# Performance work log

Hardware: AMD Instinct MI355X
Metric: run time of the kernel (lower is better)

## Reference

```python
import jax, jax.numpy as jnp
import numpy as np

D_IN = 1024
D_OUT = 1024
H = 16


def setup_inputs() -> dict:
    key = jax.random.key(0)
    ks = jax.random.split(key, 11)
    B, Tq, Tk = 2, 2048, 2048
    s = 1.0 / np.sqrt(D_IN)
    return {
        "q": jax.random.normal(ks[0], (B, Tq, D_IN), jnp.float32),
        "k": jax.random.normal(ks[1], (B, Tk, D_IN), jnp.float32),
        "v": jax.random.normal(ks[2], (B, Tk, D_IN), jnp.float32),
        "Wq": jax.random.uniform(ks[3], (D_IN, D_OUT), jnp.float32, -s, s),
        "bq": jax.random.uniform(ks[4], (D_OUT,), jnp.float32, -s, s),
        "Wk": jax.random.uniform(ks[5], (D_IN, D_OUT), jnp.float32, -s, s),
        "bk": jax.random.uniform(ks[6], (D_OUT,), jnp.float32, -s, s),
        "Wv": jax.random.uniform(ks[7], (D_IN, D_OUT), jnp.float32, -s, s),
        "bv": jax.random.uniform(ks[8], (D_OUT,), jnp.float32, -s, s),
        "Wo": jax.random.uniform(ks[9], (D_OUT, D_OUT), jnp.float32, -s, s),
        "bo": jax.random.uniform(ks[10], (D_OUT,), jnp.float32, -s, s),
    }


def reference(q, k, v, Wq, bq, Wk, bk, Wv, bv, Wo, bo):
    B, Tq, _ = q.shape
    Tk = k.shape[1]
    hd = D_OUT // H
    # QKV projections, split heads -> [B, H, T, hd]
    qh = (q @ Wq + bq).reshape(B, Tq, H, hd).transpose(0, 2, 1, 3)
    kh = (k @ Wk + bk).reshape(B, Tk, H, hd).transpose(0, 2, 1, 3)
    vh = (v @ Wv + bv).reshape(B, Tk, H, hd).transpose(0, 2, 1, 3)
    # scaled dot-product attention (scale uses key dim = head_dim)
    scores = jnp.einsum("bhqd,bhkd->bhqk", qh, kh) / jnp.sqrt(jnp.float32(hd))
    attn = jax.nn.softmax(scores, axis=-1)
    x = jnp.einsum("bhqk,bhkd->bhqd", attn, vh)
    x = x.transpose(0, 2, 1, 3).reshape(B, Tq, D_OUT)
    return x @ Wo + bo
```

## Files before the change

kernel.cpp:

```cpp
#include <hip/hip_runtime.h>
#include <hip/hip_bf16.h>

typedef __attribute__((ext_vector_type(8))) short short8;
typedef __attribute__((ext_vector_type(4))) short short4v;
typedef __attribute__((ext_vector_type(4))) float f32x4;

__device__ __forceinline__ unsigned short f2bf(float f) {
    __hip_bfloat16 h = __float2bfloat16(f);
    unsigned short u;
    __builtin_memcpy(&u, &h, 2);
    return u;
}
__device__ __forceinline__ short4v pack4bf(float a, float b, float c, float d) {
    union { unsigned u[2]; short4v s; } r;
    r.u[0] = ((unsigned)f2bf(b) << 16) | f2bf(a);
    r.u[1] = ((unsigned)f2bf(d) << 16) | f2bf(c);
    return r.s;
}

#define GLD16(gp, lp) __builtin_amdgcn_global_load_lds( \
    (const __attribute__((address_space(1))) void*)(gp), \
    (__attribute__((address_space(3))) void*)(lp), 16, 0, 0)

__global__ __launch_bounds__(256) void convert3(
    const float* __restrict__ q, const float* __restrict__ k, const float* __restrict__ v,
    unsigned short* __restrict__ qb, unsigned short* __restrict__ kb, unsigned short* __restrict__ vb)
{
    const float* src; unsigned short* dst;
    switch (blockIdx.y) { case 0: src = q; dst = qb; break;
                          case 1: src = k; dst = kb; break;
                          default: src = v; dst = vb; break; }
    size_t i = ((size_t)blockIdx.x * 256 + threadIdx.x) * 8;
    float4 x0 = *(const float4*)&src[i];
    float4 x1 = *(const float4*)&src[i + 4];
    union { unsigned short s[8]; uint4 u; } p;
    p.s[0] = f2bf(x0.x); p.s[1] = f2bf(x0.y); p.s[2] = f2bf(x0.z); p.s[3] = f2bf(x0.w);
    p.s[4] = f2bf(x1.x); p.s[5] = f2bf(x1.y); p.s[6] = f2bf(x1.z); p.s[7] = f2bf(x1.w);
    *(uint4*)&dst[i] = p.u;
}

__global__ __launch_bounds__(256) void transpose_w(
    const float* __restrict__ W0, const float* __restrict__ W1,
    const float* __restrict__ W2, const float* __restrict__ W3,
    unsigned short* __restrict__ T0, unsigned short* __restrict__ T1,
    unsigned short* __restrict__ T2, unsigned short* __restrict__ T3)
{
    __shared__ unsigned short Ts[64 * 72];
    const float* W;
    unsigned short* T;
    switch (blockIdx.z) {
        case 0: W = W0; T = T0; break;
        case 1: W = W1; T = T1; break;
        case 2: W = W2; T = T2; break;
        default: W = W3; T = T3; break;
    }
    int tid = threadIdx.x;
    int c = tid & 7, r = tid >> 3;
    int k0 = blockIdx.x * 64, n0 = blockIdx.y * 64;
    for (int i = 0; i < 64; i += 32) {
        const float* src = &W[(size_t)(k0 + r + i) * 1024 + n0 + c * 8];
        float4 x0 = *(const float4*)src;
        float4 x1 = *(const float4*)(src + 4);
        unsigned short* d = &Ts[(r + i) * 72 + c * 8];
        d[0] = f2bf(x0.x); d[1] = f2bf(x0.y); d[2] = f2bf(x0.z); d[3] = f2bf(x0.w);
        d[4] = f2bf(x1.x); d[5] = f2bf(x1.y); d[6] = f2bf(x1.z); d[7] = f2bf(x1.w);
    }
    __syncthreads();
    for (int i = 0; i < 64; i += 32) {
        union { unsigned short s[8]; uint4 v; } u;
        for (int j = 0; j < 8; j++) u.s[j] = Ts[(c * 8 + j) * 72 + (r + i)];
        *(uint4*)&T[(size_t)(n0 + r + i) * 1024 + k0 + c * 8] = u.v;
    }
}

__device__ __forceinline__ void gemm_core(
    const unsigned short* __restrict__ A, const unsigned short* __restrict__ BT,
    const float* __restrict__ bias, void* __restrict__ outv,
    int mode, float scale)
{
    const int K = 1024;
    __shared__ unsigned short As[2][128 * 32];
    __shared__ unsigned short Bs[2][128 * 32];
    int tid = threadIdx.x;
    int m0 = blockIdx.x * 128, n0 = blockIdx.y * 128;
    int lane = tid & 63, wave = tid >> 6;
    int lm = lane & 15, quad = lane >> 4;
    int wm = (wave >> 1) * 64, wn = (wave & 1) * 64;

    int lrow = lane >> 2, lcol = (lane & 3) * 8;
    const unsigned short* Ag = A + (size_t)(m0 + wave * 32 + lrow) * K + lcol;
    const unsigned short* Bg = BT + (size_t)(n0 + wave * 32 + lrow) * K + lcol;

    f32x4 acc[4][4];
    for (int i = 0; i < 4; i++)
        for (int j = 0; j < 4; j++)
            for (int r = 0; r < 4; r++) acc[i][j][r] = 0.0f;

    GLD16(Ag,          &As[0][(wave * 32) * 32]);
    GLD16(Ag + 16 * K, &As[0][(wave * 32 + 16) * 32]);
    GLD16(Bg,          &Bs[0][(wave * 32) * 32]);
    GLD16(Bg + 16 * K, &Bs[0][(wave * 32 + 16) * 32]);
    __syncthreads();

    for (int it = 0; it < 32; it++) {
        int cur = it & 1;
        if (it < 31) {
            int nxt = cur ^ 1;
            const unsigned short* Agn = Ag + (it + 1) * 32;
            const unsigned short* Bgn = Bg + (it + 1) * 32;
            GLD16(Agn,          &As[nxt][(wave * 32) * 32]);
            GLD16(Agn + 16 * K, &As[nxt][(wave * 32 + 16) * 32]);
            GLD16(Bgn,          &Bs[nxt][(wave * 32) * 32]);
            GLD16(Bgn + 16 * K, &Bs[nxt][(wave * 32 + 16) * 32]);
        }
        short8 a[4], b[4];
        for (int i = 0; i < 4; i++)
            a[i] = *(const short8*)&As[cur][(wm + i * 16 + lm) * 32 + quad * 8];
        for (int j = 0; j < 4; j++)
            b[j] = *(const short8*)&Bs[cur][(wn + j * 16 + lm) * 32 + quad * 8];
        for (int i = 0; i < 4; i++)
            for (int j = 0; j < 4; j++)
                acc[i][j] = __builtin_amdgcn_mfma_f32_16x16x32_bf16(a[i], b[j], acc[i][j], 0, 0, 0);
        __syncthreads();
    }

    for (int j = 0; j < 4; j++) {
        int col = n0 + wn + j * 16 + lm;
        float bv = bias[col];
        for (int i = 0; i < 4; i++) {
            int rowb = m0 + wm + i * 16 + quad * 4;
            if (mode == 0) {
                float* out32 = (float*)outv;
                for (int r = 0; r < 4; r++)
                    out32[(size_t)(rowb + r) * 1024 + col] = (acc[i][j][r] + bv) * scale;
            } else if (mode == 1) {
                unsigned short* out16 = (unsigned short*)outv;
                int h = col >> 6, d = col & 63;
                int bb = rowb >> 11, t = rowb & 2047;
                size_t base = (((size_t)(bb * 16 + h)) * 2048 + t) * 64 + d;
                for (int r = 0; r < 4; r++)
                    out16[base + (size_t)r * 64] = f2bf((acc[i][j][r] + bv) * scale);
            } else {
                unsigned short* out16 = (unsigned short*)outv;
                int h = col >> 6, d = col & 63;
                int bb = rowb >> 11, t = rowb & 2047;
                ushort4 pk;
                pk.x = f2bf((acc[i][j][0] + bv) * scale);
                pk.y = f2bf((acc[i][j][1] + bv) * scale);
                pk.z = f2bf((acc[i][j][2] + bv) * scale);
                pk.w = f2bf((acc[i][j][3] + bv) * scale);
                *(ushort4*)&out16[(((size_t)(bb * 16 + h)) * 64 + d) * 2048 + t] = pk;
            }
        }
    }
}

__global__ __launch_bounds__(256) void qkv_gemm(
    const unsigned short* __restrict__ qbf, const unsigned short* __restrict__ kbf,
    const unsigned short* __restrict__ vbf,
    const unsigned short* __restrict__ WqT, const unsigned short* __restrict__ WkT,
    const unsigned short* __restrict__ WvT,
    const float* __restrict__ bq, const float* __restrict__ bk, const float* __restrict__ bv,
    unsigned short* __restrict__ Qh, unsigned short* __restrict__ Kh,
    unsigned short* __restrict__ VhT)
{
    switch (blockIdx.z) {
        case 0:  gemm_core(qbf, WqT, bq, Qh,  1, 0.18033688011f); break;
        case 1:  gemm_core(kbf, WkT, bk, Kh,  1, 1.0f);           break;
        default: gemm_core(vbf, WvT, bv, VhT, 2, 1.0f);           break;
    }
}

__global__ __launch_bounds__(256) void out_gemm(
    const unsigned short* __restrict__ X, const unsigned short* __restrict__ WoT,
    const float* __restrict__ bo, float* __restrict__ out)
{
    gemm_core(X, WoT, bo, out, 0, 1.0f);
}

__global__ __launch_bounds__(256) void attn_kernel(
    const unsigned short* __restrict__ Qh, const unsigned short* __restrict__ Kh,
    const unsigned short* __restrict__ VhT, unsigned short* __restrict__ X)
{
    __shared__ unsigned short Ks[2][64 * 64];
    __shared__ unsigned short Vt[2][64 * 64];

    int tid = threadIdx.x;
    int qb = blockIdx.x & 31, bh = blockIdx.x >> 5;
    int b = bh >> 4, h = bh & 15;
    int lane = tid & 63, wave = tid >> 6;
    int lm = lane & 15, quad = lane >> 4;

    const unsigned short* Kbase = Kh + (size_t)bh * 2048 * 64;
    const unsigned short* Vbase = VhT + (size_t)bh * 64 * 2048;

    int srow = wave * 8 + (lane >> 3);
    int schk = ((lane & 7) ^ ((lane >> 3) & 7)) * 8;
    int swz  = lm & 7;
    int c0 = (quad ^ swz) * 8;
    int c1 = ((quad + 4) ^ swz) * 8;

    int qrow = qb * 64 + wave * 16 + lm;
    const unsigned short* qptr = Qh + ((size_t)bh * 2048 + qrow) * 64;
    short8 qf0 = *(const short8*)&qptr[quad * 8];
    short8 qf1 = *(const short8*)&qptr[32 + quad * 8];

    f32x4 o[4];
    for (int n = 0; n < 4; n++)
        for (int r = 0; r < 4; r++) o[n][r] = 0.0f;
    float l = 0.0f;

    GLD16(&Kbase[(size_t)srow * 64 + schk],          &Ks[0][(wave * 8) * 64]);
    GLD16(&Kbase[(size_t)(32 + srow) * 64 + schk],   &Ks[0][(32 + wave * 8) * 64]);
    GLD16(&Vbase[(size_t)srow * 2048 + schk],        &Vt[0][(wave * 8) * 64]);
    GLD16(&Vbase[(size_t)(32 + srow) * 2048 + schk], &Vt[0][(32 + wave * 8) * 64]);
    __syncthreads();

    for (int kt = 0; kt < 32; kt++) {
        int cur = kt & 1;
        if (kt < 31) {
            int k1 = (kt + 1) * 64;
            int nxt = cur ^ 1;
            GLD16(&Kbase[(size_t)(k1 + srow) * 64 + schk],        &Ks[nxt][(wave * 8) * 64]);
            GLD16(&Kbase[(size_t)(k1 + 32 + srow) * 64 + schk],   &Ks[nxt][(32 + wave * 8) * 64]);
            GLD16(&Vbase[(size_t)srow * 2048 + k1 + schk],        &Vt[nxt][(wave * 8) * 64]);
            GLD16(&Vbase[(size_t)(32 + srow) * 2048 + k1 + schk], &Vt[nxt][(32 + wave * 8) * 64]);
        }

        short4v pa[4];
        for (int t = 0; t < 4; t++) {
            short8 ka0 = *(const short8*)&Ks[cur][(t * 16 + lm) * 64 + c0];
            short8 ka1 = *(const short8*)&Ks[cur][(t * 16 + lm) * 64 + c1];
            f32x4 z;
            z[0] = z[1] = z[2] = z[3] = 0.0f;
            z = __builtin_amdgcn_mfma_f32_16x16x32_bf16(ka0, qf0, z, 0, 0, 0);
            z = __builtin_amdgcn_mfma_f32_16x16x32_bf16(ka1, qf1, z, 0, 0, 0);
            float p0 = __builtin_amdgcn_exp2f(z[0]);
            float p1 = __builtin_amdgcn_exp2f(z[1]);
            float p2 = __builtin_amdgcn_exp2f(z[2]);
            float p3 = __builtin_amdgcn_exp2f(z[3]);
            l += (p0 + p1) + (p2 + p3);
            pa[t] = pack4bf(p0, p1, p2, p3);
        }

        int wo = (quad & 1) * 4;
        for (int n = 0; n < 4; n++) {
            int rbase = (n * 16 + lm) * 64;
            for (int t = 0; t < 4; t++) {
                int chunk = t * 2 + (quad >> 1);
                short4v vb = *(const short4v*)&Vt[cur][rbase + ((chunk ^ swz) * 8) + wo];
                o[n] = __builtin_amdgcn_mfma_f32_16x16x16bf16_1k(pa[t], vb, o[n], 0, 0, 0);
            }
        }
        __syncthreads();
    }

    l += __shfl_xor(l, 16);
    l += __shfl_xor(l, 32);
    float inv = 1.0f / l;

    for (int r = 0; r < 4; r++) {
        float invr = __shfl(inv, (lane & 48) | (quad * 4 + r));
        int row = qb * 64 + wave * 16 + quad * 4 + r;
        for (int n = 0; n < 4; n++)
            X[((size_t)b * 2048 + row) * 1024 + h * 64 + n * 16 + lm] = f2bf(o[n][r] * invr);
    }
}

extern "C" void kernel_launch(void* const* d_in, const int* in_sizes, int n_in,
                              void* d_out, int out_size, void* d_ws, size_t ws_size,
                              hipStream_t stream)
{
    const float* q  = (const float*)d_in[0];
    const float* k  = (const float*)d_in[1];
    const float* v  = (const float*)d_in[2];
    const float* Wq = (const float*)d_in[3];
    const float* bq = (const float*)d_in[4];
    const float* Wk = (const float*)d_in[5];
    const float* bk = (const float*)d_in[6];
    const float* Wv = (const float*)d_in[7];
    const float* bv = (const float*)d_in[8];
    const float* Wo = (const float*)d_in[9];
    const float* bo = (const float*)d_in[10];

    unsigned short* ws  = (unsigned short*)d_ws;
    const unsigned int M1 = 1u << 20;
    unsigned short* WqT = ws;
    unsigned short* WkT = ws + M1;
    unsigned short* WvT = ws + 2 * M1;
    unsigned short* WoT = ws + 3 * M1;
    unsigned short* qbf = ws + 4 * M1;
    unsigned short* kbf = ws + 8 * M1;
    unsigned short* vbf = ws + 12 * M1;
    unsigned short* Qh  = ws + 16 * M1;
    unsigned short* Kh  = ws + 4 * M1;
    unsigned short* VhT = ws + 8 * M1;
    unsigned short* X   = ws + 12 * M1;

    convert3<<<dim3(2048, 3), 256, 0, stream>>>(q, k, v, qbf, kbf, vbf);
    transpose_w<<<dim3(16, 16, 4), 256, 0, stream>>>(Wq, Wk, Wv, Wo, WqT, WkT, WvT, WoT);
    qkv_gemm<<<dim3(32, 8, 3), 256, 0, stream>>>(qbf, kbf, vbf, WqT, WkT, WvT,
                                                 bq, bk, bv, Qh, Kh, VhT);
    attn_kernel<<<dim3(1024), 256, 0, stream>>>(Qh, Kh, VhT, X);
    out_gemm<<<dim3(32, 8), 256, 0, stream>>>(X, WoT, bo, (float*)d_out);
}
```

Baseline: 247.7 us.

## Merge prep kernels and swizzle single-buffered GEMM shared-memory tiles

Fuses the bf16 input conversion and weight transpose into one launch using a flattened block index. In the GEMM core, drops LDS double buffering for a single buffer and XOR-swizzles the 16-byte column chunks on both the global-to-LDS write and the fragment read, to avoid LDS bank conflicts. Halving LDS may allow more resident blocks per CU, but loads are no longer prefetched while MFMAs run, so global latency is exposed every K-step.

```diff
diff --git a/kernel.cpp b/kernel.cpp
--- a/kernel.cpp
+++ b/kernel.cpp
@@ -22,33 +22,36 @@
     (const __attribute__((address_space(1))) void*)(gp), \
     (__attribute__((address_space(3))) void*)(lp), 16, 0, 0)
 
-__global__ __launch_bounds__(256) void convert3(
+__global__ __launch_bounds__(256) void prep(
     const float* __restrict__ q, const float* __restrict__ k, const float* __restrict__ v,
-    unsigned short* __restrict__ qb, unsigned short* __restrict__ kb, unsigned short* __restrict__ vb)
-{
-    const float* src; unsigned short* dst;
-    switch (blockIdx.y) { case 0: src = q; dst = qb; break;
-                          case 1: src = k; dst = kb; break;
-                          default: src = v; dst = vb; break; }
-    size_t i = ((size_t)blockIdx.x * 256 + threadIdx.x) * 8;
-    float4 x0 = *(const float4*)&src[i];
-    float4 x1 = *(const float4*)&src[i + 4];
-    union { unsigned short s[8]; uint4 u; } p;
-    p.s[0] = f2bf(x0.x); p.s[1] = f2bf(x0.y); p.s[2] = f2bf(x0.z); p.s[3] = f2bf(x0.w);
-    p.s[4] = f2bf(x1.x); p.s[5] = f2bf(x1.y); p.s[6] = f2bf(x1.z); p.s[7] = f2bf(x1.w);
-    *(uint4*)&dst[i] = p.u;
-}
-
-__global__ __launch_bounds__(256) void transpose_w(
+    unsigned short* __restrict__ qb, unsigned short* __restrict__ kb, unsigned short* __restrict__ vb,
     const float* __restrict__ W0, const float* __restrict__ W1,
     const float* __restrict__ W2, const float* __restrict__ W3,
     unsigned short* __restrict__ T0, unsigned short* __restrict__ T1,
     unsigned short* __restrict__ T2, unsigned short* __restrict__ T3)
 {
     __shared__ unsigned short Ts[64 * 72];
+    int bx = blockIdx.x;
+    if (bx < 6144) {
+        const float* src; unsigned short* dst;
+        switch (bx >> 11) { case 0: src = q; dst = qb; break;
+                            case 1: src = k; dst = kb; break;
+                            default: src = v; dst = vb; break; }
+        size_t i = ((size_t)(bx & 2047) * 256 + threadIdx.x) * 8;
+        float4 x0 = *(const float4*)&src[i];
+        float4 x1 = *(const float4*)&src[i + 4];
+        union { unsigned short s[8]; uint4 u; } p;
+        p.s[0] = f2bf(x0.x); p.s[1] = f2bf(x0.y); p.s[2] = f2bf(x0.z); p.s[3] = f2bf(x0.w);
+        p.s[4] = f2bf(x1.x); p.s[5] = f2bf(x1.y); p.s[6] = f2bf(x1.z); p.s[7] = f2bf(x1.w);
+        *(uint4*)&dst[i] = p.u;
+        return;
+    }
+    int w = bx - 6144;
+    int z = w >> 8, rem = w & 255;
+    int kx = rem >> 4, ny = rem & 15;
     const float* W;
     unsigned short* T;
-    switch (blockIdx.z) {
+    switch (z) {
         case 0: W = W0; T = T0; break;
         case 1: W = W1; T = T1; break;
         case 2: W = W2; T = T2; break;
@@ -56,7 +59,7 @@
     }
     int tid = threadIdx.x;
     int c = tid & 7, r = tid >> 3;
-    int k0 = blockIdx.x * 64, n0 = blockIdx.y * 64;
+    int k0 = kx * 64, n0 = ny * 64;
     for (int i = 0; i < 64; i += 32) {
         const float* src = &W[(size_t)(k0 + r + i) * 1024 + n0 + c * 8];
         float4 x0 = *(const float4*)src;
@@ -79,45 +82,42 @@
     int mode, float scale)
 {
     const int K = 1024;
-    __shared__ unsigned short As[2][128 * 32];
-    __shared__ unsigned short Bs[2][128 * 32];
+    __shared__ unsigned short As[128 * 32];
+    __shared__ unsigned short Bs[128 * 32];
     int tid = threadIdx.x;
     int m0 = blockIdx.x * 128, n0 = blockIdx.y * 128;
     int lane = tid & 63, wave = tid >> 6;
     int lm = lane & 15, quad = lane >> 4;
     int wm = (wave >> 1) * 64, wn = (wave & 1) * 64;
 
-    int lrow = lane >> 2, lcol = (lane & 3) * 8;
-    const unsigned short* Ag = A + (size_t)(m0 + wave * 32 + lrow) * K + lcol;
-    const unsigned short* Bg = BT + (size_t)(n0 + wave * 32 + lrow) * K + lcol;
+    int lrow = lane >> 2;
+    int scol = ((lane & 3) ^ ((lane >> 3) & 3)) * 8;
+    const unsigned short* Ag = A + (size_t)(m0 + wave * 32 + lrow) * K + scol;
+    const unsigned short* Bg = BT + (size_t)(n0 + wave * 32 + lrow) * K + scol;
+    unsigned short* AsW0 = &As[(wave * 32) * 32];
+    unsigned short* AsW1 = &As[(wave * 32 + 16) * 32];
+    unsigned short* BsW0 = &Bs[(wave * 32) * 32];
+    unsigned short* BsW1 = &Bs[(wave * 32 + 16) * 32];
+
+    int rpos = (quad ^ ((lm >> 1) & 3)) * 8;
 
     f32x4 acc[4][4];
     for (int i = 0; i < 4; i++)
         for (int j = 0; j < 4; j++)
             for (int r = 0; r < 4; r++) acc[i][j][r] = 0.0f;
 
-    GLD16(Ag,          &As[0][(wave * 32) * 32]);
-    GLD16(Ag + 16 * K, &As[0][(wave * 32 + 16) * 32]);
-    GLD16(Bg,          &Bs[0][(wave * 32) * 32]);
-    GLD16(Bg + 16 * K, &Bs[0][(wave * 32 + 16) * 32]);
-    __syncthreads();
-
-    for (int it = 0; it < 32; it++) {
-        int cur = it & 1;
-        if (it < 31) {
-            int nxt = cur ^ 1;
-            const unsigned short* Agn = Ag + (it + 1) * 32;
-            const unsigned short* Bgn = Bg + (it + 1) * 32;
-            GLD16(Agn,          &As[nxt][(wave * 32) * 32]);
-            GLD16(Agn + 16 * K, &As[nxt][(wave * 32 + 16) * 32]);
-            GLD16(Bgn,          &Bs[nxt][(wave * 32) * 32]);
-            GLD16(Bgn + 16 * K, &Bs[nxt][(wave * 32 + 16) * 32]);
-        }
+    for (int kb = 0; kb < K; kb += 32) {
+        GLD16(Ag, AsW0);
+        GLD16(Ag + 16 * K, AsW1);
+        GLD16(Bg, BsW0);
+        GLD16(Bg + 16 * K, BsW1);
+        Ag += 32; Bg += 32;
+        __syncthreads();
         short8 a[4], b[4];
         for (int i = 0; i < 4; i++)
-            a[i] = *(const short8*)&As[cur][(wm + i * 16 + lm) * 32 + quad * 8];
+            a[i] = *(const short8*)&As[(wm + i * 16 + lm) * 32 + rpos];
         for (int j = 0; j < 4; j++)
-            b[j] = *(const short8*)&Bs[cur][(wn + j * 16 + lm) * 32 + quad * 8];
+            b[j] = *(const short8*)&Bs[(wn + j * 16 + lm) * 32 + rpos];
         for (int i = 0; i < 4; i++)
             for (int j = 0; j < 4; j++)
                 acc[i][j] = __builtin_amdgcn_mfma_f32_16x16x32_bf16(a[i], b[j], acc[i][j], 0, 0, 0);
@@ -297,8 +297,8 @@
     unsigned short* VhT = ws + 8 * M1;
     unsigned short* X   = ws + 12 * M1;
 
-    convert3<<<dim3(2048, 3), 256, 0, stream>>>(q, k, v, qbf, kbf, vbf);
-    transpose_w<<<dim3(16, 16, 4), 256, 0, stream>>>(Wq, Wk, Wv, Wo, WqT, WkT, WvT, WoT);
+    prep<<<dim3(7168), 256, 0, stream>>>(q, k, v, qbf, kbf, vbf,
+                                         Wq, Wk, Wv, Wo, WqT, WkT, WvT, WoT);
     qkv_gemm<<<dim3(32, 8, 3), 256, 0, stream>>>(qbf, kbf, vbf, WqT, WkT, WvT,
                                                  bq, bk, bv, Qh, Kh, VhT);
     attn_kernel<<<dim3(1024), 256, 0, stream>>>(Qh, Kh, VhT, X);
```

New measurement: 235.6 us. 1.05x faster.
